# Performance work log

Hardware: AMD Instinct MI355X
Metric: run time of the kernel (lower is better)

## Reference

```python
import jax, jax.numpy as jnp
import numpy as np

N_NODES = 100000
N_EDGES = 800000
N_GRAPHS = 128
D_IN = 84          # num_features_xd
D_HID = 840        # num_features_xd * 10
D_FC1 = 1024
D_OUT = 384


def setup_inputs() -> dict:
    key = jax.random.key(0)
    ks = jax.random.split(key, 12)
    x = jax.random.normal(ks[0], (N_NODES, D_IN), jnp.float32)
    edge_index = jax.random.randint(ks[1], (2, N_EDGES), 0, N_NODES)
    batch = jnp.sort(jax.random.randint(ks[2], (N_NODES,), 0, N_GRAPHS))

    def lin(k, fan_in, fan_out):
        bound = 1.0 / np.sqrt(fan_in)
        kw, kb = jax.random.split(k)
        W = jax.random.uniform(kw, (fan_in, fan_out), jnp.float32, -bound, bound)
        b = jax.random.uniform(kb, (fan_out,), jnp.float32, -bound, bound)
        return W, b

    W1, b1 = lin(ks[3], D_IN, D_IN)       # conv1.nn: Linear(84, 84)
    W2, b2 = lin(ks[4], D_IN, D_HID)      # conv2.nn: Linear(84, 840)
    Wg1, bg1 = lin(ks[5], 2 * D_HID, D_FC1)  # fc_g[0]: Linear(1680, 1024)
    Wg2, bg2 = lin(ks[6], D_FC1, D_OUT)      # fc_g[3]: Linear(1024, 384)
    return {"x": x, "edge_index": edge_index, "batch": batch,
            "W1": W1, "b1": b1, "W2": W2, "b2": b2,
            "Wg1": Wg1, "bg1": bg1, "Wg2": Wg2, "bg2": bg2}


def gin_conv(h, src, dst, W, b):
    # GINConv with eps=0: nn(x + sum_{j in N(i)} x_j), scatter-add over edges
    agg = jax.ops.segment_sum(h[src], dst, num_segments=N_NODES)
    return (h + agg) @ W + b


def reference(x, edge_index, batch, W1, b1, W2, b2, Wg1, bg1, Wg2, bg2):
    src, dst = edge_index[0], edge_index[1]
    h = jax.nn.relu(gin_conv(x, src, dst, W1, b1))    # [N, 84]
    h = jax.nn.relu(gin_conv(h, src, dst, W2, b2))    # [N, 840]

    # global max pool + global mean pool per graph
    counts = jax.ops.segment_sum(jnp.ones((N_NODES, 1), h.dtype), batch,
                                 num_segments=N_GRAPHS)          # [G, 1]
    sums = jax.ops.segment_sum(h, batch, num_segments=N_GRAPHS)  # [G, 840]
    meanp = sums / jnp.maximum(counts, 1.0)
    maxp = jax.ops.segment_max(h, batch, num_segments=N_GRAPHS)
    maxp = jnp.where(counts > 0, maxp, 0.0)

    z = jnp.concatenate([maxp, meanp], axis=1)        # [G, 1680]
    z = jax.nn.relu(z @ Wg1 + bg1)                    # dropout is identity in eval
    z = z @ Wg2 + bg2                                 # [G, 384]
    return z
```

## Files before the change

### kernel.cpp

```cpp
#include <hip/hip_runtime.h>

#define N_NODES 100000
#define N_EDGESC 800000
#define NGRAPH 128
#define DIN 84
#define DHID 840
#define DF1 1024
#define DOUTC 384
#define PBLK2 782
#define KP1 1696
#define NBUCK 391
#define EPB 8192
#define XSTR 96

typedef __attribute__((ext_vector_type(4))) float f32x4;
typedef __attribute__((ext_vector_type(8))) short bf16x8;

__device__ __forceinline__ unsigned short f2bf(float f) {
  union { float f; unsigned int u; } v; v.f = f;
  unsigned int r = v.u + 0x7FFFu + ((v.u >> 16) & 1u);
  return (unsigned short)(r >> 16);
}
__device__ __forceinline__ float bf2f(unsigned short h) {
  union { unsigned int u; float f; } v; v.u = ((unsigned int)h) << 16;
  return v.f;
}

__global__ __launch_bounds__(256) void k_bhist(const int* __restrict__ dst, int* __restrict__ bcnt) {
  __shared__ int h[NBUCK];
  int t = threadIdx.x;
  for (int i = t; i < NBUCK; i += 256) h[i] = 0;
  __syncthreads();
  int base = blockIdx.x * EPB;
  int e1 = min(base + EPB, N_EDGESC);
  for (int e = base + t; e < e1; e += 256)
    atomicAdd(&h[dst[e] >> 8], 1);
  __syncthreads();
  for (int i = t; i < NBUCK; i += 256) if (h[i]) atomicAdd(&bcnt[i], h[i]);
}

__global__ __launch_bounds__(512) void k_bscan(const int* __restrict__ bcnt, int* __restrict__ boff,
                                               int* __restrict__ bcur) {
  __shared__ int sd[512];
  int t = threadIdx.x;
  int v = (t < NBUCK) ? bcnt[t] : 0;
  sd[t] = v; __syncthreads();
  for (int off = 1; off < 512; off <<= 1) {
    int add = (t >= off) ? sd[t - off] : 0;
    __syncthreads();
    sd[t] += add;
    __syncthreads();
  }
  if (t <= NBUCK) {
    boff[t] = sd[t] - v;
    if (t < NBUCK) bcur[t] = sd[t] - v;
  }
}

__global__ __launch_bounds__(256) void k_bfill(const int* __restrict__ src, const int* __restrict__ dst,
                                               int* __restrict__ bcur, unsigned int* __restrict__ rec) {
  __shared__ int hcnt[NBUCK];
  __shared__ int hbase[NBUCK];
  int t = threadIdx.x;
  int e0 = blockIdx.x * EPB;
  int e1 = min(e0 + EPB, N_EDGESC);
  for (int i = t; i < NBUCK; i += 256) hcnt[i] = 0;
  __syncthreads();
  for (int e = e0 + t; e < e1; e += 256)
    atomicAdd(&hcnt[dst[e] >> 8], 1);
  __syncthreads();
  for (int i = t; i < NBUCK; i += 256) {
    int c = hcnt[i];
    hbase[i] = c ? atomicAdd(&bcur[i], c) : 0;
  }
  __syncthreads();
  for (int i = t; i < NBUCK; i += 256) hcnt[i] = 0;
  __syncthreads();
  for (int e = e0 + t; e < e1; e += 256) {
    int d = dst[e];
    int b = d >> 8;
    int r = atomicAdd(&hcnt[b], 1);
    rec[hbase[b] + r] = ((unsigned int)(d & 255) << 24) | (unsigned int)src[e];
  }
}

__global__ __launch_bounds__(256) void k_bsort(const unsigned int* __restrict__ rec, const int* __restrict__ boff,
                                               int* __restrict__ rowptr, int* __restrict__ csr) {
  __shared__ int lcnt[256];
  __shared__ int lcur[256];
  int b = blockIdx.x, t = threadIdx.x;
  int e0 = boff[b], e1 = boff[b + 1];
  lcnt[t] = 0;
  __syncthreads();
  for (int i = e0 + t; i < e1; i += 256) atomicAdd(&lcnt[rec[i] >> 24], 1);
  __syncthreads();
  int v = lcnt[t];
  for (int off = 1; off < 256; off <<= 1) {
    int add = (t >= off) ? lcnt[t - off] : 0;
    __syncthreads();
    lcnt[t] += add;
    __syncthreads();
  }
  int excl = lcnt[t] - v;
  int node = b * 256 + t;
  if (node < N_NODES) rowptr[node] = e0 + excl;
  lcur[t] = e0 + excl;
  if (b == NBUCK - 1 && t == 0) rowptr[N_NODES] = N_EDGESC;
  __syncthreads();
  for (int i = e0 + t; i < e1; i += 256) {
    unsigned int r = rec[i];
    int d = r >> 24;
    int pos = atomicAdd(&lcur[d], 1);
    csr[pos] = (int)(r & 0xFFFFFFu);
  }
}

__global__ __launch_bounds__(256) void k_counts(const int* __restrict__ batch, int* __restrict__ cnt) {
  __shared__ int h[NGRAPH];
  int t = threadIdx.x;
  if (t < NGRAPH) h[t] = 0;
  __syncthreads();
  int base = blockIdx.x * 2048;
  for (int j = 0; j < 8; j++) {
    int i = base + j * 256 + t;
    if (i < N_NODES) atomicAdd(&h[batch[i]], 1);
  }
  __syncthreads();
  if (t < NGRAPH && h[t] > 0) atomicAdd(&cnt[t], h[t]);
}

__global__ __launch_bounds__(256) void k_xbf(const float* __restrict__ x, unsigned short* __restrict__ xb) {
  int idx = blockIdx.x * 256 + threadIdx.x;
  if (idx >= N_NODES * 24) return;
  int r = idx / 24, c = idx - r * 24;
  uint2 p = {0u, 0u};
  if (c < 21) {
    f32x4 v = *(const f32x4*)&x[r * DIN + c * 4];
    p.x = (unsigned int)f2bf(v.x) | ((unsigned int)f2bf(v.y) << 16);
    p.y = (unsigned int)f2bf(v.z) | ((unsigned int)f2bf(v.w) << 16);
  }
  *(uint2*)&xb[r * XSTR + c * 4] = p;
}

__device__ __forceinline__ f32x4 bfq(uint2 p) {
  f32x4 r;
  r.x = bf2f((unsigned short)(p.x & 0xffff)); r.y = bf2f((unsigned short)(p.x >> 16));
  r.z = bf2f((unsigned short)(p.y & 0xffff)); r.w = bf2f((unsigned short)(p.y >> 16));
  return r;
}

__global__ __launch_bounds__(256) void k_agg1b(const unsigned short* __restrict__ xb, const int* __restrict__ rowptr,
                                               const int* __restrict__ csr, float* __restrict__ out) {
  int node = blockIdx.x * 8 + (threadIdx.x >> 5);
  int lane = threadIdx.x & 31;
  if (node >= N_NODES) return;
  int r0 = rowptr[node], r1 = rowptr[node + 1];
  bool act = lane < 21;
  f32x4 a = {0.f, 0.f, 0.f, 0.f};
  if (act) a = bfq(*(const uint2*)&xb[node * XSTR + lane * 4]);
  int e = r0;
  for (; e + 4 <= r1; e += 4) {
    int s0 = csr[e], s1 = csr[e + 1], s2 = csr[e + 2], s3 = csr[e + 3];
    if (act) {
      uint2 q0 = *(const uint2*)&xb[s0 * XSTR + lane * 4];
      uint2 q1 = *(const uint2*)&xb[s1 * XSTR + lane * 4];
      uint2 q2 = *(const uint2*)&xb[s2 * XSTR + lane * 4];
      uint2 q3 = *(const uint2*)&xb[s3 * XSTR + lane * 4];
      a += (bfq(q0) + bfq(q1)) + (bfq(q2) + bfq(q3));
    }
  }
  for (; e < r1; e++) {
    int s = csr[e];
    if (act) a += bfq(*(const uint2*)&xb[s * XSTR + lane * 4]);
  }
  if (act) ((f32x4*)out)[node * 21 + lane] = a;
}

__global__ __launch_bounds__(256) void k_agg2(const unsigned short* __restrict__ h1b, const int* __restrict__ rowptr,
                                              const int* __restrict__ csr, unsigned short* __restrict__ out) {
  int node = blockIdx.x * 8 + (threadIdx.x >> 5);
  int lane = threadIdx.x & 31;
  if (node >= N_NODES) return;
  int r0 = rowptr[node], r1 = rowptr[node + 1];
  bool act = lane < 21;
  f32x4 a = {0.f, 0.f, 0.f, 0.f};
  if (act) a = bfq(*(const uint2*)&h1b[node * XSTR + lane * 4]);
  int e = r0;
  for (; e + 4 <= r1; e += 4) {
    int s0 = csr[e], s1 = csr[e + 1], s2 = csr[e + 2], s3 = csr[e + 3];
    if (act) {
      uint2 q0 = *(const uint2*)&h1b[s0 * XSTR + lane * 4];
      uint2 q1 = *(const uint2*)&h1b[s1 * XSTR + lane * 4];
      uint2 q2 = *(const uint2*)&h1b[s2 * XSTR + lane * 4];
      uint2 q3 = *(const uint2*)&h1b[s3 * XSTR + lane * 4];
      a += (bfq(q0) + bfq(q1)) + (bfq(q2) + bfq(q3));
    }
  }
  for (; e < r1; e++) {
    int s = csr[e];
    if (act) a += bfq(*(const uint2*)&h1b[s * XSTR + lane * 4]);
  }
  if (lane < 24) {
    uint2 p;
    if (act) {
      p.x = (unsigned int)f2bf(a.x) | ((unsigned int)f2bf(a.y) << 16);
      p.y = (unsigned int)f2bf(a.z) | ((unsigned int)f2bf(a.w) << 16);
    } else {
      p.x = 0u; p.y = 0u;
    }
    *(uint2*)&out[node * XSTR + lane * 4] = p;
  }
}

__global__ __launch_bounds__(256) void k_w1t(const float* __restrict__ W1, unsigned short* __restrict__ w1h,
                                             unsigned short* __restrict__ w1l) {
  int idx = blockIdx.x * 256 + threadIdx.x;
  if (idx >= 96 * 96) return;
  int n = idx / 96, k = idx % 96;
  float v = (n < DIN && k < DIN) ? W1[k * DIN + n] : 0.f;
  unsigned short h = f2bf(v);
  w1h[idx] = h;
  w1l[idx] = f2bf(v - bf2f(h));
}

template <int K, int KPAD, int N>
__global__ __launch_bounds__(256) void k_wsplit(const float* __restrict__ W,
                                                unsigned short* __restrict__ wh,
                                                unsigned short* __restrict__ wl) {
  __shared__ float tile[32][33];
  int b = blockIdx.x;
  int kt = b % (KPAD / 32), nt = b / (KPAD / 32);
  int k0 = kt * 32, n0 = nt * 32;
  int t = threadIdx.x;
  int r = t >> 3, c4 = (t & 7) * 4;
  int k = k0 + r;
  f32x4 v = {0.f, 0.f, 0.f, 0.f};
  if (k < K) v = *(const f32x4*)&W[(size_t)k * N + n0 + c4];
  tile[r][c4 + 0] = v.x; tile[r][c4 + 1] = v.y; tile[r][c4 + 2] = v.z; tile[r][c4 + 3] = v.w;
  __syncthreads();
  int n = t >> 3;
  float f0 = tile[c4 + 0][n], f1 = tile[c4 + 1][n], f2 = tile[c4 + 2][n], f3 = tile[c4 + 3][n];
  unsigned short h0 = f2bf(f0), h1_ = f2bf(f1), h2_ = f2bf(f2), h3_ = f2bf(f3);
  uint2 ph, pl;
  ph.x = (unsigned int)h0 | ((unsigned int)h1_ << 16);
  ph.y = (unsigned int)h2_ | ((unsigned int)h3_ << 16);
  pl.x = (unsigned int)f2bf(f0 - bf2f(h0)) | ((unsigned int)f2bf(f1 - bf2f(h1_)) << 16);
  pl.y = (unsigned int)f2bf(f2 - bf2f(h2_)) | ((unsigned int)f2bf(f3 - bf2f(h3_)) << 16);
  *(uint2*)&wh[(size_t)(n0 + n) * KPAD + k0 + c4] = ph;
  *(uint2*)&wl[(size_t)(n0 + n) * KPAD + k0 + c4] = pl;
}

__global__ __launch_bounds__(256) void k_conv1m(const float* __restrict__ agg,
                                                const unsigned short* __restrict__ w1h,
                                                const unsigned short* __restrict__ w1l,
                                                const float* __restrict__ b1,
                                                unsigned short* __restrict__ h1b) {
  constexpr int LDA = 104;
  __shared__ __align__(16) unsigned short Ah[64 * LDA];
  __shared__ __align__(16) unsigned short Al[64 * LDA];
  int t = threadIdx.x;
  int m0 = blockIdx.x * 64;

  for (int idx = t; idx < 64 * 21; idx += 256) {
    int r = idx / 21, c = idx - r * 21;
    int row = m0 + r;
    f32x4 v = {0.f, 0.f, 0.f, 0.f};
    if (row < N_NODES) v = *(const f32x4*)&agg[row * DIN + c * 4];
    unsigned short h0 = f2bf(v.x), h1_ = f2bf(v.y), h2_ = f2bf(v.z), h3_ = f2bf(v.w);
    unsigned short l0 = f2bf(v.x - bf2f(h0)), l1 = f2bf(v.y - bf2f(h1_));
    unsigned short l2 = f2bf(v.z - bf2f(h2_)), l3 = f2bf(v.w - bf2f(h3_));
    unsigned int* ph = (unsigned int*)&Ah[r * LDA + c * 4];
    ph[0] = (unsigned int)h0 | ((unsigned int)h1_ << 16);
    ph[1] = (unsigned int)h2_ | ((unsigned int)h3_ << 16);
    unsigned int* pl = (unsigned int*)&Al[r * LDA + c * 4];
    pl[0] = (unsigned int)l0 | ((unsigned int)l1 << 16);
    pl[1] = (unsigned int)l2 | ((unsigned int)l3 << 16);
  }
  for (int idx = t; idx < 64 * 6; idx += 256) {
    int r = idx / 6, c = idx - r * 6;
    ((unsigned int*)&Ah[r * LDA + 84])[c] = 0;
    ((unsigned int*)&Al[r * LDA + 84])[c] = 0;
  }
  __syncthreads();

  int w = t >> 6, l = t & 63;
  int lr = l & 15, lk = (l >> 4) * 8;
  bf16x8 ah[3], al[3];
  #pragma unroll
  for (int kk = 0; kk < 3; kk++) {
    ah[kk] = *(bf16x8*)&Ah[(w * 16 + lr) * LDA + lk + kk * 32];
    al[kk] = *(bf16x8*)&Al[(w * 16 + lr) * LDA + lk + kk * 32];
  }

  #pragma unroll
  for (int nt = 0; nt < 6; nt++) {
    f32x4 acc = {0.f, 0.f, 0.f, 0.f};
    #pragma unroll
    for (int kk = 0; kk < 3; kk++) {
      bf16x8 bh = *(const bf16x8*)&w1h[(nt * 16 + lr) * 96 + lk + kk * 32];
      bf16x8 bl = *(const bf16x8*)&w1l[(nt * 16 + lr) * 96 + lk + kk * 32];
      acc = __builtin_amdgcn_mfma_f32_16x16x32_bf16(ah[kk], bh, acc, 0, 0, 0);
      acc = __builtin_amdgcn_mfma_f32_16x16x32_bf16(al[kk], bh, acc, 0, 0, 0);
      acc = __builtin_amdgcn_mfma_f32_16x16x32_bf16(ah[kk], bl, acc, 0, 0, 0);
    }
    int col = nt * 16 + lr;
    if (col < DIN) {
      float bias = b1[col];
      int rbase = m0 + w * 16 + (l >> 4) * 4;
      #pragma unroll
      for (int j = 0; j < 4; j++) {
        if (rbase + j < N_NODES)
          h1b[(rbase + j) * XSTR + col] = f2bf(fmaxf(acc[j] + bias, 0.f));
      }
    }
  }
}

__global__ __launch_bounds__(256) void k_w2t(const float* __restrict__ W2, unsigned short* __restrict__ w2t) {
  int idx = blockIdx.x * 256 + threadIdx.x;
  if (idx >= 896 * 96) return;
  int n = idx / 96, k = idx % 96;
  float v = (n < DHID && k < DIN) ? W2[k * DHID + n] : 0.f;
  w2t[idx] = f2bf(v);
}

__global__ __launch_bounds__(256) void k_conv2pool3(const unsigned short* __restrict__ aggb,
                                                    const unsigned short* __restrict__ w2t,
                                                    const float* __restrict__ b2,
                                                    const int* __restrict__ batch,
                                                    int* __restrict__ pm0, float* __restrict__ ps0,
                                                    int* __restrict__ pm1, float* __restrict__ ps1,
                                                    int* __restrict__ blkg,
                                                    int* __restrict__ maxb, float* __restrict__ sump) {
  __shared__ int   smax0[DHID]; __shared__ float ssum0[DHID];
  __shared__ int   smax1[DHID]; __shared__ float ssum1[DHID];
  int t = threadIdx.x;
  int w = t >> 6, l = t & 63;
  int b = blockIdx.x;
  int m0 = b * 128;
  int r0 = m0 + (w & 1) * 64;
  int lr = l & 15, hi = l >> 4, lk = hi * 8;

  for (int i = t; i < DHID; i += 256) { smax0[i] = 0; ssum0[i] = 0.f; smax1[i] = 0; ssum1[i] = 0.f; }

  bf16x8 afr[4][3];
  #pragma unroll
  for (int rg = 0; rg < 4; rg++) {
    int row = r0 + rg * 16 + lr;
    #pragma unroll
    for (int kk = 0; kk < 3; kk++) {
      bf16x8 v = {0, 0, 0, 0, 0, 0, 0, 0};
      if (row < N_NODES) v = *(const bf16x8*)&aggb[row * XSTR + lk + kk * 32];
      afr[rg][kk] = v;
    }
  }

  int g0 = batch[m0];
  int g1 = batch[min(m0 + 127, N_NODES - 1)];
  bool fast = (g0 == g1) && (m0 + 127 < N_NODES);
  __syncthreads();

  if (fast) {
    for (int nc = (w >> 1); nc < 14; nc += 2) {
      #pragma unroll
      for (int nt = 0; nt < 4; nt++) {
        int c = nc * 64 + nt * 16 + lr;
        const unsigned short* bp = &w2t[(nc * 64 + nt * 16 + lr) * 96 + lk];
        bf16x8 b0v = *(const bf16x8*)(bp);
        bf16x8 b1v = *(const bf16x8*)(bp + 32);
        bf16x8 b2v = *(const bf16x8*)(bp + 64);
        float bias = (c < DHID) ? b2[c] : 0.f;
        float mx = 0.f, sm = 0.f;
        #pragma unroll
        for (int rg = 0; rg < 4; rg++) {
          f32x4 a_ = {0.f, 0.f, 0.f, 0.f};
          a_ = __builtin_amdgcn_mfma_f32_16x16x32_bf16(afr[rg][0], b0v, a_, 0, 0, 0);
          a_ = __builtin_amdgcn_mfma_f32_16x16x32_bf16(afr[rg][1], b1v, a_, 0, 0, 0);
          a_ = __builtin_amdgcn_mfma_f32_16x16x32_bf16(afr[rg][2], b2v, a_, 0, 0, 0);
          #pragma unroll
          for (int j = 0; j < 4; j++) {
            float v = fmaxf(a_[j] + bias, 0.f);
            mx = fmaxf(mx, v); sm += v;
          }
        }
        mx = fmaxf(mx, __shfl_xor(mx, 16)); sm += __shfl_xor(sm, 16);
        mx = fmaxf(mx, __shfl_xor(mx, 32)); sm += __shfl_xor(sm, 32);
        if (hi == 0 && c < DHID) {
          atomicMax(&smax0[c], __float_as_int(mx));
          atomicAdd(&ssum0[c], sm);
        }
      }
    }
  } else {
    int grow[4][4];
    #pragma unroll
    for (int rg = 0; rg < 4; rg++)
      #pragma unroll
      for (int j = 0; j < 4; j++) {
        int row = r0 + rg * 16 + hi * 4 + j;
        grow[rg][j] = (row < N_NODES) ? batch[row] : -1;
      }
    for (int nc = (w >> 1); nc < 14; nc += 2) {
      #pragma unroll
      for (int nt = 0; nt < 4; nt++) {
        int c = nc * 64 + nt * 16 + lr;
        const unsigned short* bp = &w2t[(nc * 64 + nt * 16 + lr) * 96 + lk];
        bf16x8 b0v = *(const bf16x8*)(bp);
        bf16x8 b1v = *(const bf16x8*)(bp + 32);
        bf16x8 b2v = *(const bf16x8*)(bp + 64);
        float bias = (c < DHID) ? b2[c] : 0.f;
        float mx0 = 0.f, sm0 = 0.f, mx1 = 0.f, sm1 = 0.f;
        float vv[4][4];
        #pragma unroll
        for (int rg = 0; rg < 4; rg++) {
          f32x4 a_ = {0.f, 0.f, 0.f, 0.f};
          a_ = __builtin_amdgcn_mfma_f32_16x16x32_bf16(afr[rg][0], b0v, a_, 0, 0, 0);
          a_ = __builtin_amdgcn_mfma_f32_16x16x32_bf16(afr[rg][1], b1v, a_, 0, 0, 0);
          a_ = __builtin_amdgcn_mfma_f32_16x16x32_bf16(afr[rg][2], b2v, a_, 0, 0, 0);
          #pragma unroll
          for (int j = 0; j < 4; j++) {
            float v = fmaxf(a_[j] + bias, 0.f);
            vv[rg][j] = v;
            if (grow[rg][j] == g0) { mx0 = fmaxf(mx0, v); sm0 += v; }
            if (grow[rg][j] == g1) { mx1 = fmaxf(mx1, v); sm1 += v; }
          }
        }
        mx0 = fmaxf(mx0, __shfl_xor(mx0, 16)); sm0 += __shfl_xor(sm0, 16);
        mx0 = fmaxf(mx0, __shfl_xor(mx0, 32)); sm0 += __shfl_xor(sm0, 32);
        mx1 = fmaxf(mx1, __shfl_xor(mx1, 16)); sm1 += __shfl_xor(sm1, 16);
        mx1 = fmaxf(mx1, __shfl_xor(mx1, 32)); sm1 += __shfl_xor(sm1, 32);
        if (hi == 0 && c < DHID) {
          atomicMax(&smax0[c], __float_as_int(mx0));
          atomicAdd(&ssum0[c], sm0);
          atomicMax(&smax1[c], __float_as_int(mx1));
          atomicAdd(&ssum1[c], sm1);
        }
        if (g1 - g0 >= 2) {
          for (int g = g0 + 1; g < g1; g++) {
            float mx = 0.f, sm = 0.f;
            #pragma unroll
            for (int rg = 0; rg < 4; rg++)
              #pragma unroll
              for (int j = 0; j < 4; j++)
                if (grow[rg][j] == g) { mx = fmaxf(mx, vv[rg][j]); sm += vv[rg][j]; }
            mx = fmaxf(mx, __shfl_xor(mx, 16)); sm += __shfl_xor(sm, 16);
            mx = fmaxf(mx, __shfl_xor(mx, 32)); sm += __shfl_xor(sm, 32);
            if (hi == 0 && c < DHID) {
              atomicMax(&maxb[g * DHID + c], __float_as_int(mx));
              atomicAdd(&sump[g * DHID + c], sm);
            }
          }
        }
      }
    }
  }
  __syncthreads();
  for (int i = t; i < DHID; i += 256) {
    pm0[b * DHID + i] = smax0[i];
    ps0[b * DHID + i] = ssum0[i];
  }
  if (g0 != g1) {
    for (int i = t; i < DHID; i += 256) {
      pm1[b * DHID + i] = smax1[i];
      ps1[b * DHID + i] = ssum1[i];
    }
  }
  if (t == 0) { blkg[b * 2] = g0; blkg[b * 2 + 1] = g1; }
}

__global__ __launch_bounds__(256) void k_pool2(const int* __restrict__ pm0, const float* __restrict__ ps0,
                                               const int* __restrict__ pm1, const float* __restrict__ ps1,
                                               const int* __restrict__ blkg, const int* __restrict__ cnt,
                                               const int* __restrict__ maxb, const float* __restrict__ sump,
                                               unsigned short* __restrict__ zh, unsigned short* __restrict__ zl) {
  __shared__ int sstart[NGRAPH];
  int g = blockIdx.x, t = threadIdx.x;
  if (t == 0) {
    int s = 0;
    for (int i = 0; i < NGRAPH; i++) { sstart[i] = s; s += cnt[i]; }
  }
  __syncthreads();
  int c0 = cnt[g];
  int ns = sstart[g], ne = ns + c0;
  int b0 = ns / 128, b1 = (c0 > 0) ? (ne - 1) / 128 : b0 - 1;
  for (int c = t; c < DHID; c += 256) {
    float mx = __int_as_float(maxb[g * DHID + c]);
    float sm = sump[g * DHID + c];
    for (int b = b0; b <= b1; b++) {
      int gg0 = blkg[2 * b], gg1 = blkg[2 * b + 1];
      if (gg0 == g)      { mx = fmaxf(mx, __int_as_float(pm0[b * DHID + c])); sm += ps0[b * DHID + c]; }
      else if (gg1 == g) { mx = fmaxf(mx, __int_as_float(pm1[b * DHID + c])); sm += ps1[b * DHID + c]; }
    }
    float vmax = (c0 > 0) ? mx : 0.f;
    float vmean = sm / (float)max(c0, 1);
    unsigned short hm = f2bf(vmax);
    zh[g * KP1 + c] = hm;
    zl[g * KP1 + c] = f2bf(vmax - bf2f(hm));
    unsigned short he = f2bf(vmean);
    zh[g * KP1 + DHID + c] = he;
    zl[g * KP1 + DHID + c] = f2bf(vmean - bf2f(he));
  }
  if (t < KP1 - 2 * DHID) {
    zh[g * KP1 + 2 * DHID + t] = 0;
    zl[g * KP1 + 2 * DHID + t] = 0;
  }
}

__global__ __launch_bounds__(256) void k_mlp1m(const unsigned short* __restrict__ zh, const unsigned short* __restrict__ zl,
                                               const unsigned short* __restrict__ wh, const unsigned short* __restrict__ wl,
                                               const float* __restrict__ bg,
                                               unsigned short* __restrict__ z1h, unsigned short* __restrict__ z1l) {
  int t = threadIdx.x, w = t >> 6, l = t & 63;
  int lr = l & 15, hi = l >> 4, lk = hi * 8;
  int b = blockIdx.x;
  int n0 = (b >> 1) * 16;
  int m0 = (b & 1) * 64 + w * 16;
  const unsigned short* za = &zh[(size_t)(m0 + lr) * KP1 + lk];
  const unsigned short* zb = &zl[(size_t)(m0 + lr) * KP1 + lk];
  const unsigned short* wa = &wh[(size_t)(n0 + lr) * KP1 + lk];
  const unsigned short* wb = &wl[(size_t)(n0 + lr) * KP1 + lk];
  f32x4 acc = {0.f, 0.f, 0.f, 0.f};
  for (int ks = 0; ks < KP1 / 32; ks++) {
    bf16x8 ah = *(const bf16x8*)(za + ks * 32);
    bf16x8 al = *(const bf16x8*)(zb + ks * 32);
    bf16x8 bh = *(const bf16x8*)(wa + ks * 32);
    bf16x8 bl = *(const bf16x8*)(wb + ks * 32);
    acc = __builtin_amdgcn_mfma_f32_16x16x32_bf16(ah, bh, acc, 0, 0, 0);
    acc = __builtin_amdgcn_mfma_f32_16x16x32_bf16(al, bh, acc, 0, 0, 0);
    acc = __builtin_amdgcn_mfma_f32_16x16x32_bf16(ah, bl, acc, 0, 0, 0);
  }
  int col = n0 + lr;
  float bias = bg[col];
  #pragma unroll
  for (int j = 0; j < 4; j++) {
    int row = m0 + hi * 4 + j;
    float v = fmaxf(acc[j] + bias, 0.f);
    unsigned short h = f2bf(v);
    z1h[row * DF1 + col] = h;
    z1l[row * DF1 + col] = f2bf(v - bf2f(h));
  }
}

__global__ __launch_bounds__(256) void k_mlp2m(const unsigned short* __restrict__ z1h, const unsigned short* __restrict__ z1l,
                                               const unsigned short* __restrict__ wh, const unsigned short* __restrict__ wl,
                                               const float* __restrict__ bg, float* __restrict__ out) {
  int t = threadIdx.x, w = t >> 6, l = t & 63;
  int lr = l & 15, hi = l >> 4, lk = hi * 8;
  int b = blockIdx.x;
  int n0 = (b >> 1) * 16;
  int m0 = (b & 1) * 64 + w * 16;
  const unsigned short* za = &z1h[(size_t)(m0 + lr) * DF1 + lk];
  const unsigned short* zb = &z1l[(size_t)(m0 + lr) * DF1 + lk];
  const unsigned short* wa = &wh[(size_t)(n0 + lr) * DF1 + lk];
  const unsigned short* wb = &wl[(size_t)(n0 + lr) * DF1 + lk];
  f32x4 acc = {0.f, 0.f, 0.f, 0.f};
  for (int ks = 0; ks < DF1 / 32; ks++) {
    bf16x8 ah = *(const bf16x8*)(za + ks * 32);
    bf16x8 al = *(const bf16x8*)(zb + ks * 32);
    bf16x8 bh = *(const bf16x8*)(wa + ks * 32);
    bf16x8 bl = *(const bf16x8*)(wb + ks * 32);
    acc = __builtin_amdgcn_mfma_f32_16x16x32_bf16(ah, bh, acc, 0, 0, 0);
    acc = __builtin_amdgcn_mfma_f32_16x16x32_bf16(al, bh, acc, 0, 0, 0);
    acc = __builtin_amdgcn_mfma_f32_16x16x32_bf16(ah, bl, acc, 0, 0, 0);
  }
  int col = n0 + lr;
  float bias = bg[col];
  #pragma unroll
  for (int j = 0; j < 4; j++) {
    int row = m0 + hi * 4 + j;
    out[row * DOUTC + col] = acc[j] + bias;
  }
}

static constexpr size_t AL(size_t x) { return (x + 255) & ~(size_t)255; }

extern "C" void kernel_launch(void* const* d_in, const int* in_sizes, int n_in,
                              void* d_out, int out_size, void* d_ws, size_t ws_size,
                              hipStream_t stream) {
  const float* x   = (const float*)d_in[0];
  const int*  edge = (const int*)d_in[1];
  const int*  batch= (const int*)d_in[2];
  const float* W1  = (const float*)d_in[3];
  const float* b1  = (const float*)d_in[4];
  const float* W2  = (const float*)d_in[5];
  const float* b2  = (const float*)d_in[6];
  const float* Wg1 = (const float*)d_in[7];
  const float* bg1 = (const float*)d_in[8];
  const float* Wg2 = (const float*)d_in[9];
  const float* bg2 = (const float*)d_in[10];
  float* out = (float*)d_out;
  const int* src = edge;
  const int* dst = edge + N_EDGESC;

  size_t o = 0;
  size_t OFF_AGG = o;  o += AL((size_t)N_NODES * DIN * 4);
  size_t OFF_H1  = o;  o += AL((size_t)N_NODES * XSTR * 2);
  size_t OFF_AGB = o;  o += AL((size_t)N_NODES * XSTR * 2);
  size_t OFF_CSR = o;  o += AL((size_t)N_EDGESC * 4);
  size_t OFF_REC = o;  o += AL((size_t)N_EDGESC * 4);
  size_t OFF_W2T = o;  o += AL((size_t)896 * 96 * 2);
  size_t OFF_W1H = o;  o += AL((size_t)96 * 96 * 2);
  size_t OFF_W1L = o;  o += AL((size_t)96 * 96 * 2);
  size_t OFF_G1H = o;  o += AL((size_t)DF1 * KP1 * 2);
  size_t OFF_G1L = o;  o += AL((size_t)DF1 * KP1 * 2);
  size_t OFF_G2H = o;  o += AL((size_t)DOUTC * DF1 * 2);
  size_t OFF_G2L = o;  o += AL((size_t)DOUTC * DF1 * 2);
  size_t OFF_ZH  = o;  o += AL((size_t)NGRAPH * KP1 * 2);
  size_t OFF_ZL  = o;  o += AL((size_t)NGRAPH * KP1 * 2);
  size_t OFF_Z1H = o;  o += AL((size_t)NGRAPH * DF1 * 2);
  size_t OFF_Z1L = o;  o += AL((size_t)NGRAPH * DF1 * 2);
  size_t OFF_RP  = o;  o += AL((size_t)(N_NODES + 1) * 4);
  size_t OFF_BOF = o;  o += AL((NBUCK + 1) * 4);
  size_t OFF_BCU = o;  o += AL(NBUCK * 4);
  size_t OFF_BC  = o;  o += AL(NBUCK * 4);
  size_t OFF_MAX = o;  o += AL((size_t)NGRAPH * DHID * 4);
  size_t OFF_SUM = o;  o += AL((size_t)NGRAPH * DHID * 4);
  size_t OFF_CNT = o;  o += AL(NGRAPH * 4);
  size_t TOTAL = o;
  size_t ZERO0 = OFF_BC, ZEROB = TOTAL - OFF_BC;
  if (ws_size < TOTAL) return;

  size_t PB = AL((size_t)PBLK2 * DHID * 4);
  size_t OFF_PM0 = OFF_AGG;
  size_t OFF_PS0 = OFF_AGG + PB;
  size_t OFF_PM1 = OFF_AGG + 2 * PB;
  size_t OFF_PS1 = OFF_AGG + 3 * PB;
  size_t OFF_BLG = OFF_AGG + 4 * PB;

  char* ws = (char*)d_ws;
  float* agg = (float*)(ws + OFF_AGG);
  unsigned short* h1b = (unsigned short*)(ws + OFF_H1);
  unsigned short* aggb = (unsigned short*)(ws + OFF_AGB);
  unsigned short* xb   = (unsigned short*)(ws + OFF_AGB);
  int* csr   = (int*)(ws + OFF_CSR);
  unsigned int* rec = (unsigned int*)(ws + OFF_REC);
  unsigned short* w2t = (unsigned short*)(ws + OFF_W2T);
  unsigned short* w1h = (unsigned short*)(ws + OFF_W1H);
  unsigned short* w1l = (unsigned short*)(ws + OFF_W1L);
  unsigned short* g1h = (unsigned short*)(ws + OFF_G1H);
  unsigned short* g1l = (unsigned short*)(ws + OFF_G1L);
  unsigned short* g2h = (unsigned short*)(ws + OFF_G2H);
  unsigned short* g2l = (unsigned short*)(ws + OFF_G2L);
  unsigned short* zh  = (unsigned short*)(ws + OFF_ZH);
  unsigned short* zl  = (unsigned short*)(ws + OFF_ZL);
  unsigned short* z1h = (unsigned short*)(ws + OFF_Z1H);
  unsigned short* z1l = (unsigned short*)(ws + OFF_Z1L);
  int* rowptr = (int*)(ws + OFF_RP);
  int* boff  = (int*)(ws + OFF_BOF);
  int* bcur  = (int*)(ws + OFF_BCU);
  int* bcnt  = (int*)(ws + OFF_BC);
  int* maxb  = (int*)(ws + OFF_MAX);
  float* sump= (float*)(ws + OFF_SUM);
  int* cnt   = (int*)(ws + OFF_CNT);
  int* pm0   = (int*)(ws + OFF_PM0);
  float* ps0 = (float*)(ws + OFF_PS0);
  int* pm1   = (int*)(ws + OFF_PM1);
  float* ps1 = (float*)(ws + OFF_PS1);
  int* blkg  = (int*)(ws + OFF_BLG);

  hipMemsetAsync(ws + ZERO0, 0, ZEROB, stream);

  k_w2t<<<(896 * 96 + 255) / 256, 256, 0, stream>>>(W2, w2t);
  k_w1t<<<(96 * 96 + 255) / 256, 256, 0, stream>>>(W1, w1h, w1l);
  k_wsplit<2 * DHID, KP1, DF1><<<(KP1 / 32) * (DF1 / 32), 256, 0, stream>>>(Wg1, g1h, g1l);
  k_wsplit<DF1, DF1, DOUTC><<<(DF1 / 32) * (DOUTC / 32), 256, 0, stream>>>(Wg2, g2h, g2l);
  k_xbf<<<(N_NODES * 24 + 255) / 256, 256, 0, stream>>>(x, xb);

  int nbb = (N_EDGESC + EPB - 1) / EPB;
  k_bhist<<<nbb, 256, 0, stream>>>(dst, bcnt);
  k_bscan<<<1, 512, 0, stream>>>(bcnt, boff, bcur);
  k_bfill<<<nbb, 256, 0, stream>>>(src, dst, bcur, rec);
  k_bsort<<<NBUCK, 256, 0, stream>>>(rec, boff, rowptr, csr);
  k_counts<<<(N_NODES + 2047) / 2048, 256, 0, stream>>>(batch, cnt);

  k_agg1b<<<(N_NODES + 7) / 8, 256, 0, stream>>>(xb, rowptr, csr, agg);
  k_conv1m<<<(N_NODES + 63) / 64, 256, 0, stream>>>(agg, w1h, w1l, b1, h1b);
  k_agg2<<<(N_NODES + 7) / 8, 256, 0, stream>>>(h1b, rowptr, csr, aggb);
  k_conv2pool3<<<PBLK2, 256, 0, stream>>>(aggb, w2t, b2, batch, pm0, ps0, pm1, ps1, blkg, maxb, sump);
  k_pool2<<<NGRAPH, 256, 0, stream>>>(pm0, ps0, pm1, ps1, blkg, cnt, maxb, sump, zh, zl);

  k_mlp1m<<<(DF1 / 16) * 2, 256, 0, stream>>>(zh, zl, g1h, g1l, bg1, z1h, z1l);
  k_mlp2m<<<(DOUTC / 16) * 2, 256, 0, stream>>>(z1h, z1l, g2h, g2l, bg2, out);
}
```

Before: 286.2 us.

## Shrink conv2-pool row tiles to 64 and write per-block partials directly

The fused conv2+pool kernel now processes 64 rows per block instead of 128, doubling the grid. Each of the four waves covers a disjoint set of column chunks, so the block-level shared-memory atomics and final copy-out are dropped. Each wave writes interleaved (max, sum) float2 partials straight to global memory. The A tile is staged through padded LDS before loading into fragments. This aims to raise parallelism and remove LDS atomic contention, at the cost of twice as many partials for the final pool reduction to read.

Measured after the change: 286.6 us. No clear change (+0.1%).

```diff
diff --git a/kernel.cpp b/kernel.cpp
--- a/kernel.cpp
+++ b/kernel.cpp
@@ -7,7 +7,7 @@
 #define DHID 840
 #define DF1 1024
 #define DOUTC 384
-#define PBLK2 782
+#define PBLK3 1563
 #define KP1 1696
 #define NBUCK 391
 #define EPB 8192
@@ -324,44 +324,42 @@
   w2t[idx] = f2bf(v);
 }
 
-__global__ __launch_bounds__(256) void k_conv2pool3(const unsigned short* __restrict__ aggb,
+__global__ __launch_bounds__(256) void k_conv2pool4(const unsigned short* __restrict__ aggb,
                                                     const unsigned short* __restrict__ w2t,
                                                     const float* __restrict__ b2,
                                                     const int* __restrict__ batch,
-                                                    int* __restrict__ pm0, float* __restrict__ ps0,
-                                                    int* __restrict__ pm1, float* __restrict__ ps1,
+                                                    float2* __restrict__ pm, float2* __restrict__ pm1,
                                                     int* __restrict__ blkg,
                                                     int* __restrict__ maxb, float* __restrict__ sump) {
-  __shared__ int   smax0[DHID]; __shared__ float ssum0[DHID];
-  __shared__ int   smax1[DHID]; __shared__ float ssum1[DHID];
+  constexpr int LDA = 104;
+  __shared__ __align__(16) unsigned short At[64 * LDA];
   int t = threadIdx.x;
   int w = t >> 6, l = t & 63;
   int b = blockIdx.x;
-  int m0 = b * 128;
-  int r0 = m0 + (w & 1) * 64;
+  int m0 = b * 64;
   int lr = l & 15, hi = l >> 4, lk = hi * 8;
 
-  for (int i = t; i < DHID; i += 256) { smax0[i] = 0; ssum0[i] = 0.f; smax1[i] = 0; ssum1[i] = 0.f; }
+  for (int idx = t; idx < 64 * 12; idx += 256) {
+    int r = idx / 12, c = idx - r * 12;
+    uint4 v = {0u, 0u, 0u, 0u};
+    int row = m0 + r;
+    if (row < N_NODES) v = *(const uint4*)&aggb[row * XSTR + c * 8];
+    *(uint4*)&At[r * LDA + c * 8] = v;
+  }
+  int g0 = batch[m0];
+  int g1 = batch[min(m0 + 63, N_NODES - 1)];
+  bool fast = (g0 == g1) && (m0 + 63 < N_NODES);
+  __syncthreads();
 
   bf16x8 afr[4][3];
   #pragma unroll
-  for (int rg = 0; rg < 4; rg++) {
-    int row = r0 + rg * 16 + lr;
+  for (int rg = 0; rg < 4; rg++)
     #pragma unroll
-    for (int kk = 0; kk < 3; kk++) {
-      bf16x8 v = {0, 0, 0, 0, 0, 0, 0, 0};
-      if (row < N_NODES) v = *(const bf16x8*)&aggb[row * XSTR + lk + kk * 32];
-      afr[rg][kk] = v;
-    }
-  }
-
-  int g0 = batch[m0];
-  int g1 = batch[min(m0 + 127, N_NODES - 1)];
-  bool fast = (g0 == g1) && (m0 + 127 < N_NODES);
-  __syncthreads();
+    for (int kk = 0; kk < 3; kk++)
+      afr[rg][kk] = *(bf16x8*)&At[(rg * 16 + lr) * LDA + lk + kk * 32];
 
   if (fast) {
-    for (int nc = (w >> 1); nc < 14; nc += 2) {
+    for (int nc = w; nc < 14; nc += 4) {
       #pragma unroll
       for (int nt = 0; nt < 4; nt++) {
         int c = nc * 64 + nt * 16 + lr;
@@ -377,18 +375,16 @@
           a_ = __builtin_amdgcn_mfma_f32_16x16x32_bf16(afr[rg][0], b0v, a_, 0, 0, 0);
           a_ = __builtin_amdgcn_mfma_f32_16x16x32_bf16(afr[rg][1], b1v, a_, 0, 0, 0);
           a_ = __builtin_amdgcn_mfma_f32_16x16x32_bf16(afr[rg][2], b2v, a_, 0, 0, 0);
-          #pragma unroll
-          for (int j = 0; j < 4; j++) {
-            float v = fmaxf(a_[j] + bias, 0.f);
-            mx = fmaxf(mx, v); sm += v;
-          }
+          float v0 = fmaxf(a_[0] + bias, 0.f);
+          float v1 = fmaxf(a_[1] + bias, 0.f);
+          float v2 = fmaxf(a_[2] + bias, 0.f);
+          float v3 = fmaxf(a_[3] + bias, 0.f);
+          mx = fmaxf(mx, fmaxf(fmaxf(v0, v1), fmaxf(v2, v3)));
+          sm += (v0 + v1) + (v2 + v3);
         }
         mx = fmaxf(mx, __shfl_xor(mx, 16)); sm += __shfl_xor(sm, 16);
         mx = fmaxf(mx, __shfl_xor(mx, 32)); sm += __shfl_xor(sm, 32);
-        if (hi == 0 && c < DHID) {
-          atomicMax(&smax0[c], __float_as_int(mx));
-          atomicAdd(&ssum0[c], sm);
-        }
+        if (hi == 0 && c < DHID) pm[(size_t)b * DHID + c] = make_float2(mx, sm);
       }
     }
   } else {
@@ -397,10 +393,10 @@
     for (int rg = 0; rg < 4; rg++)
       #pragma unroll
       for (int j = 0; j < 4; j++) {
-        int row = r0 + rg * 16 + hi * 4 + j;
+        int row = m0 + rg * 16 + hi * 4 + j;
         grow[rg][j] = (row < N_NODES) ? batch[row] : -1;
       }
-    for (int nc = (w >> 1); nc < 14; nc += 2) {
+    for (int nc = w; nc < 14; nc += 4) {
       #pragma unroll
       for (int nt = 0; nt < 4; nt++) {
         int c = nc * 64 + nt * 16 + lr;
@@ -430,10 +426,8 @@
         mx1 = fmaxf(mx1, __shfl_xor(mx1, 16)); sm1 += __shfl_xor(sm1, 16);
         mx1 = fmaxf(mx1, __shfl_xor(mx1, 32)); sm1 += __shfl_xor(sm1, 32);
         if (hi == 0 && c < DHID) {
-          atomicMax(&smax0[c], __float_as_int(mx0));
-          atomicAdd(&ssum0[c], sm0);
-          atomicMax(&smax1[c], __float_as_int(mx1));
-          atomicAdd(&ssum1[c], sm1);
+          pm[(size_t)b * DHID + c] = make_float2(mx0, sm0);
+          pm1[(size_t)b * DHID + c] = make_float2(mx1, sm1);
         }
         if (g1 - g0 >= 2) {
           for (int g = g0 + 1; g < g1; g++) {
@@ -454,22 +448,10 @@
       }
     }
   }
-  __syncthreads();
-  for (int i = t; i < DHID; i += 256) {
-    pm0[b * DHID + i] = smax0[i];
-    ps0[b * DHID + i] = ssum0[i];
-  }
-  if (g0 != g1) {
-    for (int i = t; i < DHID; i += 256) {
-      pm1[b * DHID + i] = smax1[i];
-      ps1[b * DHID + i] = ssum1[i];
-    }
-  }
   if (t == 0) { blkg[b * 2] = g0; blkg[b * 2 + 1] = g1; }
 }
 
-__global__ __launch_bounds__(256) void k_pool2(const int* __restrict__ pm0, const float* __restrict__ ps0,
-                                               const int* __restrict__ pm1, const float* __restrict__ ps1,
+__global__ __launch_bounds__(256) void k_pool2(const float2* __restrict__ pm, const float2* __restrict__ pm1,
                                                const int* __restrict__ blkg, const int* __restrict__ cnt,
                                                const int* __restrict__ maxb, const float* __restrict__ sump,
                                                unsigned short* __restrict__ zh, unsigned short* __restrict__ zl) {
@@ -482,14 +464,14 @@
   __syncthreads();
   int c0 = cnt[g];
   int ns = sstart[g], ne = ns + c0;
-  int b0 = ns / 128, b1 = (c0 > 0) ? (ne - 1) / 128 : b0 - 1;
+  int b0 = ns / 64, b1 = (c0 > 0) ? (ne - 1) / 64 : b0 - 1;
   for (int c = t; c < DHID; c += 256) {
     float mx = __int_as_float(maxb[g * DHID + c]);
     float sm = sump[g * DHID + c];
     for (int b = b0; b <= b1; b++) {
       int gg0 = blkg[2 * b], gg1 = blkg[2 * b + 1];
-      if (gg0 == g)      { mx = fmaxf(mx, __int_as_float(pm0[b * DHID + c])); sm += ps0[b * DHID + c]; }
-      else if (gg1 == g) { mx = fmaxf(mx, __int_as_float(pm1[b * DHID + c])); sm += ps1[b * DHID + c]; }
+      if (gg0 == g)      { float2 p = pm[(size_t)b * DHID + c];  mx = fmaxf(mx, p.x); sm += p.y; }
+      else if (gg1 == g) { float2 p = pm1[(size_t)b * DHID + c]; mx = fmaxf(mx, p.x); sm += p.y; }
     }
     float vmax = (c0 > 0) ? mx : 0.f;
     float vmean = sm / (float)max(c0, 1);
@@ -620,12 +602,10 @@
   size_t ZERO0 = OFF_BC, ZEROB = TOTAL - OFF_BC;
   if (ws_size < TOTAL) return;
 
-  size_t PB = AL((size_t)PBLK2 * DHID * 4);
-  size_t OFF_PM0 = OFF_AGG;
-  size_t OFF_PS0 = OFF_AGG + PB;
-  size_t OFF_PM1 = OFF_AGG + 2 * PB;
-  size_t OFF_PS1 = OFF_AGG + 3 * PB;
-  size_t OFF_BLG = OFF_AGG + 4 * PB;
+  size_t PB = AL((size_t)PBLK3 * DHID * 8);
+  size_t OFF_PM  = OFF_AGG;
+  size_t OFF_PM1 = OFF_AGG + PB;
+  size_t OFF_BLG = OFF_AGG + 2 * PB;
 
   char* ws = (char*)d_ws;
   float* agg = (float*)(ws + OFF_AGG);
@@ -652,10 +632,8 @@
   int* maxb  = (int*)(ws + OFF_MAX);
   float* sump= (float*)(ws + OFF_SUM);
   int* cnt   = (int*)(ws + OFF_CNT);
-  int* pm0   = (int*)(ws + OFF_PM0);
-  float* ps0 = (float*)(ws + OFF_PS0);
-  int* pm1   = (int*)(ws + OFF_PM1);
-  float* ps1 = (float*)(ws + OFF_PS1);
+  float2* pm  = (float2*)(ws + OFF_PM);
+  float2* pm1 = (float2*)(ws + OFF_PM1);
   int* blkg  = (int*)(ws + OFF_BLG);
 
   hipMemsetAsync(ws + ZERO0, 0, ZEROB, stream);
@@ -676,8 +654,8 @@
   k_agg1b<<<(N_NODES + 7) / 8, 256, 0, stream>>>(xb, rowptr, csr, agg);
   k_conv1m<<<(N_NODES + 63) / 64, 256, 0, stream>>>(agg, w1h, w1l, b1, h1b);
   k_agg2<<<(N_NODES + 7) / 8, 256, 0, stream>>>(h1b, rowptr, csr, aggb);
-  k_conv2pool3<<<PBLK2, 256, 0, stream>>>(aggb, w2t, b2, batch, pm0, ps0, pm1, ps1, blkg, maxb, sump);
-  k_pool2<<<NGRAPH, 256, 0, stream>>>(pm0, ps0, pm1, ps1, blkg, cnt, maxb, sump, zh, zl);
+  k_conv2pool4<<<PBLK3, 256, 0, stream>>>(aggb, w2t, b2, batch, pm, pm1, blkg, maxb, sump);
+  k_pool2<<<NGRAPH, 256, 0, stream>>>(pm, pm1, blkg, cnt, maxb, sump, zh, zl);
 
   k_mlp1m<<<(DF1 / 16) * 2, 256, 0, stream>>>(zh, zl, g1h, g1l, bg1, z1h, z1l);
   k_mlp2m<<<(DOUTC / 16) * 2, 256, 0, stream>>>(z1h, z1l, g2h, g2l, bg2, out);
```
